# Optimization experiments

Measured on AMD Instinct MI355X. Metric: run time of the kernel, lower is better.

Reference implementation:

```python
import jax, jax.numpy as jnp
import numpy as np

K = 20  # top-K neighbors per stock
SLOPE = 0.2  # LeakyReLU negative slope


def _gru_layer(x, Wih, Whh, bih, bhh):
    # x: [N, T, D]; PyTorch GRU gate order: r, z, n
    H = Whh.shape[1]
    def step(h, xt):
        gi = xt @ Wih.T + bih            # [N, 3H]
        gh = h @ Whh.T + bhh             # [N, 3H]
        ir, iz, inn = jnp.split(gi, 3, axis=1)
        hr, hz, hn = jnp.split(gh, 3, axis=1)
        r = jax.nn.sigmoid(ir + hr)
        z = jax.nn.sigmoid(iz + hz)
        n = jnp.tanh(inn + r * hn)
        h_new = (1.0 - z) * n + z * h
        return h_new, h_new
    h0 = jnp.zeros((x.shape[0], H), x.dtype)
    _, ys = jax.lax.scan(step, h0, jnp.swapaxes(x, 0, 1))
    return jnp.swapaxes(ys, 0, 1)        # [N, T, H]


def _cos_sim(x, y):
    # torch: xy / (||x|| ||y||^T), NaN (0/0) replaced by 0
    xy = x @ y.T
    xn = jnp.sqrt(jnp.sum(x * x, axis=1, keepdims=True))
    yn = jnp.sqrt(jnp.sum(y * y, axis=1, keepdims=True))
    denom = xn @ yn.T
    safe = jnp.where(denom == 0.0, 1.0, denom)
    return jnp.where(denom == 0.0, 0.0, xy / safe)


def setup_inputs() -> dict:
    key = jax.random.key(0)
    ks = jax.random.split(key, 20)
    N, T, F, H = 4096, 64, 32, 128
    def rn(k, shape, scale=0.1):
        return jax.random.normal(k, shape, dtype=jnp.float32) * scale
    b01 = lambda n: jnp.full((n,), 0.1, jnp.float32)
    return {
        'x': jax.random.normal(ks[0], (N, T, F), dtype=jnp.float32),
        'Wih0': rn(ks[1], (3 * H, F)), 'Whh0': rn(ks[2], (3 * H, H)),
        'bih0': rn(ks[3], (3 * H,)), 'bhh0': rn(ks[4], (3 * H,)),
        'Wih1': rn(ks[5], (3 * H, H)), 'Whh1': rn(ks[6], (3 * H, H)),
        'bih1': rn(ks[7], (3 * H,)), 'bhh1': rn(ks[8], (3 * H,)),
        'W_hc': rn(ks[9], (H, H)), 'b_hc': b01(H),
        'W_hs': rn(ks[10], (H, H)), 'b_hs': b01(H),
        'W_fore': rn(ks[11], (H, H)), 'b_fore': b01(H),
        'W_back': rn(ks[12], (H, H)), 'b_back': b01(H),
        'W_indi': rn(ks[13], (H, H)), 'b_indi': b01(H),
        'W_out': rn(ks[14], (1, H)), 'b_out': b01(1),
    }


def reference(x, Wih0, Whh0, bih0, bhh0, Wih1, Whh1, bih1, bhh1,
              W_hc, b_hc, W_hs, b_hs, W_fore, b_fore, W_back, b_back,
              W_indi, b_indi, W_out, b_out):
    lrelu = lambda v: jax.nn.leaky_relu(v, SLOPE)
    h = _gru_layer(x, Wih0, Whh0, bih0, bhh0)
    h = _gru_layer(h, Wih1, Whh1, bih1, bhh1)
    g = h[:, -1, :]                                   # [N, H] last-step GRU output
    N = g.shape[0]

    sim = _cos_sim(g, g)                              # [N, N]
    diag = jnp.diagonal(sim)
    sim_off = sim * (1.0 - jnp.eye(N, dtype=sim.dtype))

    # top-K (by |sim|) neighbor mask via scatter
    cols = jax.lax.top_k(jnp.abs(sim_off), K)[1]      # [N, K]
    rows = jnp.repeat(jnp.arange(N), K)
    mask = jnp.zeros((N, N), sim.dtype).at[rows, cols.reshape(-1)].set(1.0)

    tks = sim_off * mask
    col_nz = (jnp.sum(tks, axis=0) != 0).astype(sim.dtype)
    tks = tks + jnp.diag(col_nz * diag)

    # concept features; zero rows (empty concepts) are masked instead of filtered
    concept_raw = tks.T @ g                           # [N, H]
    valid = (jnp.sum(concept_raw, axis=1) != 0).astype(g.dtype)
    cf = lrelu(concept_raw @ W_hc.T + b_hc) * valid[:, None]

    attn = jax.nn.softmax(_cos_sim(g, cf), axis=0)    # softmax over stocks per concept
    hs = lrelu((attn @ cf) @ W_hs.T + b_hs)
    back = lrelu(hs @ W_back.T + b_back)
    fore = lrelu(hs @ W_fore.T + b_fore)
    indi = lrelu((g - back) @ W_indi.T + b_indi)
    pred = (fore + indi) @ W_out.T + b_out            # [N, 1]
    return pred.squeeze(-1)
```

## Files before the change

### kernel.cpp

```cpp
#include <hip/hip_runtime.h>
#include <hip/hip_bf16.h>


typedef float f32x4 __attribute__((ext_vector_type(4)));
typedef short s16x8 __attribute__((ext_vector_type(8)));
typedef unsigned short u16;
typedef unsigned long long u64;

#define DEVFN static __device__ __forceinline__

DEVFN u16 f2bf(float f) {
  union { float f; unsigned u; } v; v.f = f;
  return (u16)((v.u + 0x7FFFu + ((v.u >> 16) & 1u)) >> 16);
}

DEVFN unsigned f2bf_pk(float lo, float hi) {
  union { __hip_bfloat162 h; unsigned u; } p;
  p.h = __float22bfloat162_rn(make_float2(lo, hi));
  return p.u;
}

DEVFN f32x4 mfma16(s16x8 a, s16x8 b, f32x4 c) {
  return __builtin_amdgcn_mfma_f32_16x16x32_bf16(a, b, c, 0, 0, 0);
}

DEVFN float sigmf(float x) { return __builtin_amdgcn_rcpf(1.f + __expf(-x)); }
DEVFN float tanhf_fast(float x) {
  float e = __expf(2.f * x);
  return 1.f - 2.f * __builtin_amdgcn_rcpf(e + 1.f);
}
DEVFN float lrelu(float v) { return v > 0.f ? v : 0.2f * v; }

__global__ void cvt_all(const float* __restrict__ w0, const float* __restrict__ w1,
                        const float* __restrict__ w2, const float* __restrict__ w3,
                        const float* __restrict__ w4, const float* __restrict__ w5,
                        const float* __restrict__ w6, const float* __restrict__ w7,
                        u16* __restrict__ dst, int* __restrict__ zbuf) {
  int i = blockIdx.x * 256 + threadIdx.x;
  if (i >= 225280) return;
  if (i < 12288) zbuf[i] = 0;
  float v;
  if      (i < 12288)  v = w0[i];
  else if (i < 61440)  v = w1[i - 12288];
  else if (i < 110592) v = w2[i - 61440];
  else if (i < 159744) v = w3[i - 110592];
  else if (i < 176128) v = w4[i - 159744];
  else if (i < 192512) v = w5[i - 176128];
  else if (i < 208896) v = w6[i - 192512];
  else                 v = w7[i - 208896];
  dst[i] = f2bf(v);
}

__launch_bounds__(512, 1)
__global__ void gru_fused(const float* __restrict__ x,
                          const u16* __restrict__ Wih0, const u16* __restrict__ Whh0,
                          const float* __restrict__ bih0, const float* __restrict__ bhh0,
                          const u16* __restrict__ Wih1, const u16* __restrict__ Whh1,
                          const float* __restrict__ bih1, const float* __restrict__ bhh1,
                          float* __restrict__ g_out, u16* __restrict__ gbf,
                          float* __restrict__ rn)
{
  const int tid  = threadIdx.x;
  const int w    = tid >> 6;
  const int l    = tid & 63;
  const int quad = l >> 4;
  const int l16  = l & 15;
  const int r0   = blockIdx.x * 16;
  const int c    = w * 16 + l16;

  __shared__ u16 sh_x[64][16 * 40];
  __shared__ u16 sh_h0[2][16 * 136];
  __shared__ u16 sh_h1[2][16 * 136];
  __shared__ float red16[16][8];

  s16x8 B0ih[3];
  s16x8 B0hh[3][4];
  s16x8 B1ih[3][4];
  s16x8 B1hh[3][4];
  float brz0[2], bin0, bhn0, brz1[2], bin1, bhn1;
  {
    int j0g = c, j1g = 128 + c, j2g = 256 + c;
    brz0[0] = bih0[j0g] + bhh0[j0g];  brz0[1] = bih0[j1g] + bhh0[j1g];
    bin0 = bih0[j2g];  bhn0 = bhh0[j2g];
    brz1[0] = bih1[j0g] + bhh1[j0g];  brz1[1] = bih1[j1g] + bhh1[j1g];
    bin1 = bih1[j2g];  bhn1 = bhh1[j2g];
  }
#pragma unroll
  for (int g = 0; g < 3; ++g) {
    int j = g * 128 + c;
    B0ih[g] = *(const s16x8*)(Wih0 + j * 32 + quad * 8);
#pragma unroll
    for (int kk = 0; kk < 4; ++kk) {
      B0hh[g][kk] = *(const s16x8*)(Whh0 + j * 128 + kk * 32 + quad * 8);
      B1ih[g][kk] = *(const s16x8*)(Wih1 + j * 128 + kk * 32 + quad * 8);
      B1hh[g][kk] = *(const s16x8*)(Whh1 + j * 128 + kk * 32 + quad * 8);
    }
  }
  float h0reg[4] = {0.f, 0.f, 0.f, 0.f};
  float h1reg[4] = {0.f, 0.f, 0.f, 0.f};
  for (int idx = tid; idx < 16 * 136; idx += 512) sh_h1[0][idx] = 0;

  for (int q = tid; q < 8192; q += 512) {
    int r  = q >> 9;
    int t  = (q >> 3) & 63;
    int c4 = (q & 7) * 4;
    float4 v = *(const float4*)(x + (size_t)(r0 + r) * 2048 + t * 32 + c4);
    unsigned p0 = f2bf_pk(v.x, v.y);
    unsigned p1 = f2bf_pk(v.z, v.w);
    *(uint2*)(&sh_x[t][r * 40 + c4]) = make_uint2(p0, p1);
  }
  __syncthreads();

  const f32x4 zz4 = {0.f, 0.f, 0.f, 0.f};
  {
    s16x8 ax = *(const s16x8*)(sh_x[0] + l16 * 40 + quad * 8);
    f32x4 ai[3];
#pragma unroll
    for (int g = 0; g < 3; ++g) ai[g] = mfma16(ax, B0ih[g], zz4);
#pragma unroll
    for (int i = 0; i < 4; i += 2) {
      float hn[2];
#pragma unroll
      for (int q = 0; q < 2; ++q) {
        int ii = i + q;
        float rr = sigmf(ai[0][ii] + brz0[0]);
        float zg = sigmf(ai[1][ii] + brz0[1]);
        float nn = tanhf_fast(ai[2][ii] + bin0 + rr * bhn0);
        hn[q] = nn - zg * nn;
        h0reg[ii] = hn[q];
      }
      unsigned pk = f2bf_pk(hn[0], hn[1]);
      int m = quad * 4 + i;
      sh_h0[0][m * 136 + c]       = (u16)pk;
      sh_h0[0][(m + 1) * 136 + c] = (u16)(pk >> 16);
    }
  }

#define GRU_STEP(T, CUR, NXT)                                                     \
  {                                                                               \
    __syncthreads();                                                              \
    s16x8 ah0[4], ah1[4];                                                         \
    _Pragma("unroll")                                                             \
    for (int kk = 0; kk < 4; ++kk) {                                              \
      ah0[kk] = *(const s16x8*)(sh_h0[CUR] + l16 * 136 + kk * 32 + quad * 8);     \
      ah1[kk] = *(const s16x8*)(sh_h1[CUR] + l16 * 136 + kk * 32 + quad * 8);     \
    }                                                                             \
    s16x8 ax = *(const s16x8*)(sh_x[(T) + 1] + l16 * 40 + quad * 8);              \
    f32x4 r1a, z1a, ni1, nh1, r0a, z0a, ni0, nh0;                                 \
    r1a = mfma16(ah0[0], B1ih[0][0], zz4);                                        \
    z1a = mfma16(ah0[0], B1ih[1][0], zz4);                                        \
    ni1 = mfma16(ah0[0], B1ih[2][0], zz4);                                        \
    nh1 = mfma16(ah1[0], B1hh[2][0], zz4);                                        \
    r0a = mfma16(ax, B0ih[0], zz4);                                               \
    z0a = mfma16(ax, B0ih[1], zz4);                                               \
    ni0 = mfma16(ax, B0ih[2], zz4);                                               \
    nh0 = mfma16(ah0[0], B0hh[2][0], zz4);                                        \
    _Pragma("unroll")                                                             \
    for (int kk = 1; kk < 4; ++kk) {                                              \
      r1a = mfma16(ah0[kk], B1ih[0][kk], r1a);                                    \
      z1a = mfma16(ah0[kk], B1ih[1][kk], z1a);                                    \
      ni1 = mfma16(ah0[kk], B1ih[2][kk], ni1);                                    \
      nh1 = mfma16(ah1[kk], B1hh[2][kk], nh1);                                    \
      nh0 = mfma16(ah0[kk], B0hh[2][kk], nh0);                                    \
    }                                                                             \
    _Pragma("unroll")                                                             \
    for (int kk = 0; kk < 4; ++kk) {                                              \
      r1a = mfma16(ah1[kk], B1hh[0][kk], r1a);                                    \
      z1a = mfma16(ah1[kk], B1hh[1][kk], z1a);                                    \
      r0a = mfma16(ah0[kk], B0hh[0][kk], r0a);                                    \
      z0a = mfma16(ah0[kk], B0hh[1][kk], z0a);                                    \
    }                                                                             \
    _Pragma("unroll")                                                             \
    for (int i = 0; i < 4; i += 2) {                                              \
      float hn[2];                                                                \
      _Pragma("unroll")                                                           \
      for (int q = 0; q < 2; ++q) {                                               \
        int ii = i + q;                                                           \
        float rr = sigmf(r1a[ii] + brz1[0]);                                      \
        float zg = sigmf(z1a[ii] + brz1[1]);                                      \
        float nn = tanhf_fast(ni1[ii] + bin1 + rr * (nh1[ii] + bhn1));            \
        hn[q] = nn + zg * (h1reg[ii] - nn);                                       \
        h1reg[ii] = hn[q];                                                        \
      }                                                                           \
      unsigned pk = f2bf_pk(hn[0], hn[1]);                                        \
      int m = quad * 4 + i;                                                       \
      sh_h1[NXT][m * 136 + c]       = (u16)pk;                                    \
      sh_h1[NXT][(m + 1) * 136 + c] = (u16)(pk >> 16);                            \
    }                                                                             \
    _Pragma("unroll")                                                             \
    for (int i = 0; i < 4; i += 2) {                                              \
      float hn[2];                                                                \
      _Pragma("unroll")                                                           \
      for (int q = 0; q < 2; ++q) {                                               \
        int ii = i + q;                                                           \
        float rr = sigmf(r0a[ii] + brz0[0]);                                      \
        float zg = sigmf(z0a[ii] + brz0[1]);                                      \
        float nn = tanhf_fast(ni0[ii] + bin0 + rr * (nh0[ii] + bhn0));            \
        hn[q] = nn + zg * (h0reg[ii] - nn);                                       \
        h0reg[ii] = hn[q];                                                        \
      }                                                                           \
      unsigned pk = f2bf_pk(hn[0], hn[1]);                                        \
      int m = quad * 4 + i;                                                       \
      sh_h0[NXT][m * 136 + c]       = (u16)pk;                                    \
      sh_h0[NXT][(m + 1) * 136 + c] = (u16)(pk >> 16);                            \
    }                                                                             \
  }

  for (int t2 = 0; t2 < 31; ++t2) {
    int t = t2 * 2;
    GRU_STEP(t, 0, 1);
    GRU_STEP(t + 1, 1, 0);
  }
  GRU_STEP(62, 0, 1);
#undef GRU_STEP

  __syncthreads();
  {
    s16x8 ah0[4], ah1[4];
#pragma unroll
    for (int kk = 0; kk < 4; ++kk) {
      ah0[kk] = *(const s16x8*)(sh_h0[1] + l16 * 136 + kk * 32 + quad * 8);
      ah1[kk] = *(const s16x8*)(sh_h1[1] + l16 * 136 + kk * 32 + quad * 8);
    }
    f32x4 r1a, z1a, ni1, nh1;
    r1a = mfma16(ah0[0], B1ih[0][0], zz4);
    z1a = mfma16(ah0[0], B1ih[1][0], zz4);
    ni1 = mfma16(ah0[0], B1ih[2][0], zz4);
    nh1 = mfma16(ah1[0], B1hh[2][0], zz4);
#pragma unroll
    for (int kk = 1; kk < 4; ++kk) {
      r1a = mfma16(ah0[kk], B1ih[0][kk], r1a);
      z1a = mfma16(ah0[kk], B1ih[1][kk], z1a);
      ni1 = mfma16(ah0[kk], B1ih[2][kk], ni1);
      nh1 = mfma16(ah1[kk], B1hh[2][kk], nh1);
    }
#pragma unroll
    for (int kk = 0; kk < 4; ++kk) {
      r1a = mfma16(ah1[kk], B1hh[0][kk], r1a);
      z1a = mfma16(ah1[kk], B1hh[1][kk], z1a);
    }
    float hv[4];
#pragma unroll
    for (int i = 0; i < 4; ++i) {
      int m = quad * 4 + i;
      float rr = sigmf(r1a[i] + brz1[0]);
      float zg = sigmf(z1a[i] + brz1[1]);
      float nn = tanhf_fast(ni1[i] + bin1 + rr * (nh1[i] + bhn1));
      float hnew = nn + zg * (h1reg[i] - nn);
      hv[i] = hnew;
      g_out[(size_t)(r0 + m) * 128 + c] = hnew;
      gbf[(size_t)(r0 + m) * 128 + c]   = f2bf(hnew);
    }
#pragma unroll
    for (int i = 0; i < 4; ++i) {
      float s = hv[i] * hv[i];
      s += __shfl_xor(s, 1);
      s += __shfl_xor(s, 2);
      s += __shfl_xor(s, 4);
      s += __shfl_xor(s, 8);
      if (l16 == 0) red16[quad * 4 + i][w] = s;
    }
  }
  __syncthreads();
  if (tid < 16) {
    float s = 0.f;
#pragma unroll
    for (int k = 0; k < 8; ++k) s += red16[tid][k];
    rn[r0 + tid] = (s == 0.f) ? 0.f : rsqrtf(s);
  }
}

template<int MODE>
__launch_bounds__(256, 1)
__global__ void cos_gemm(const u16* __restrict__ A, const u16* __restrict__ B,
                         const float* __restrict__ rnA, const float* __restrict__ rnB,
                         float* __restrict__ C, u16* __restrict__ E,
                         float* __restrict__ colsum)
{
  __shared__ u16 shA[128 * 136];
  __shared__ u16 shB[128 * 136];
  const int tid = threadIdx.x;
  const int l = tid & 63, wv = tid >> 6;
  const int quad = l >> 4, l16 = l & 15;
  const int i0 = blockIdx.y * 128, j0 = blockIdx.x * 128;
  {
    int r = tid >> 1, half = tid & 1;
    const int4* sa = (const int4*)(A + (size_t)(i0 + r) * 128 + half * 64);
    int4* da = (int4*)(shA + r * 136 + half * 64);
    const int4* sb = (const int4*)(B + (size_t)(j0 + r) * 128 + half * 64);
    int4* db = (int4*)(shB + r * 136 + half * 64);
#pragma unroll
    for (int q = 0; q < 8; ++q) { da[q] = sa[q]; db[q] = sb[q]; }
  }
  __syncthreads();
  const int wm = wv >> 1, wn = wv & 1;
  f32x4 acc[4][4];
  const f32x4 zz4 = {0.f, 0.f, 0.f, 0.f};
#pragma unroll
  for (int a = 0; a < 4; ++a)
#pragma unroll
    for (int b = 0; b < 4; ++b) acc[a][b] = zz4;
#pragma unroll
  for (int kk = 0; kk < 4; ++kk) {
    s16x8 af[4], bfr[4];
#pragma unroll
    for (int mt = 0; mt < 4; ++mt)
      af[mt] = *(const s16x8*)(shA + (wm * 64 + mt * 16 + l16) * 136 + kk * 32 + quad * 8);
#pragma unroll
    for (int nt = 0; nt < 4; ++nt)
      bfr[nt] = *(const s16x8*)(shB + (wn * 64 + nt * 16 + l16) * 136 + kk * 32 + quad * 8);
#pragma unroll
    for (int mt = 0; mt < 4; ++mt)
#pragma unroll
      for (int nt = 0; nt < 4; ++nt) acc[mt][nt] = mfma16(af[mt], bfr[nt], acc[mt][nt]);
  }
  float ra[4][4];
#pragma unroll
  for (int mt = 0; mt < 4; ++mt)
#pragma unroll
    for (int i = 0; i < 4; ++i) ra[mt][i] = rnA[i0 + wm * 64 + mt * 16 + quad * 4 + i];
#pragma unroll
  for (int nt = 0; nt < 4; ++nt) {
    int col = j0 + wn * 64 + nt * 16 + l16;
    float rb = rnB[col];
    float psum = 0.f;
#pragma unroll
    for (int mt = 0; mt < 4; ++mt)
#pragma unroll
      for (int i = 0; i < 4; ++i) {
        int row = i0 + wm * 64 + mt * 16 + quad * 4 + i;
        float v = acc[mt][nt][i] * ra[mt][i] * rb;
        if constexpr (MODE == 0) {
          C[(size_t)row * 4096 + col] = v;
        } else {
          float e = __expf(v);
          E[(size_t)row * 4096 + col] = f2bf(e);
          psum += e;
        }
      }
    if constexpr (MODE == 1) {
      psum += __shfl_xor(psum, 16);
      psum += __shfl_xor(psum, 32);
      if (quad == 0) atomicAdd(colsum + col, psum);
    }
  }
}

__launch_bounds__(256, 1)
__global__ void topk_select(const float* __restrict__ sim,
                            int* __restrict__ gselj, float* __restrict__ gselv,
                            int* __restrict__ cnt, int* __restrict__ touched)
{
  __shared__ unsigned hist[2048];
  __shared__ u64 cand[3072];
  __shared__ int selj[20];
  __shared__ unsigned ws4[4];
  __shared__ int shb, shcnt;
  const int tid = threadIdx.x;
  const int row = blockIdx.x;
  const int l = tid & 63, wv = tid >> 6;

  for (int i = tid; i < 2048; i += 256) hist[i] = 0;
  if (tid == 0) shcnt = 0;
  __syncthreads();

  unsigned key[4][4];
#pragma unroll
  for (int q = 0; q < 4; ++q) {
    int e0 = (q * 256 + tid) * 4;
    float4 v = *(const float4*)(sim + (size_t)row * 4096 + e0);
    key[q][0] = (e0 + 0 == row) ? 0u : (__float_as_uint(v.x) & 0x7FFFFFFFu);
    key[q][1] = (e0 + 1 == row) ? 0u : (__float_as_uint(v.y) & 0x7FFFFFFFu);
    key[q][2] = (e0 + 2 == row) ? 0u : (__float_as_uint(v.z) & 0x7FFFFFFFu);
    key[q][3] = (e0 + 3 == row) ? 0u : (__float_as_uint(v.w) & 0x7FFFFFFFu);
#pragma unroll
    for (int c = 0; c < 4; ++c) {
      unsigned bin = key[q][c] >> 19; if (bin > 2047u) bin = 2047u;
      atomicAdd(&hist[bin], 1u);
    }
  }
  __syncthreads();

  unsigned s = 0;
#pragma unroll
  for (int j = 0; j < 8; ++j) s += hist[tid * 8 + j];
  unsigned r = s;
#pragma unroll
  for (int off = 1; off < 64; off <<= 1) {
    unsigned o = __shfl_down(r, off);
    if (l + off < 64) r += o;
  }
  if (l == 0) ws4[wv] = r;
  __syncthreads();
  unsigned upper = 0;
  for (int q = wv + 1; q < 4; ++q) upper += ws4[q];
  unsigned excl = upper + (r - s);
  if (excl < 20u && excl + s >= 20u) {
    unsigned cum = excl;
    for (int j = 7; j >= 0; --j) {
      cum += hist[tid * 8 + j];
      if (cum >= 20u) { shb = tid * 8 + j; break; }
    }
  }
  __syncthreads();
  const unsigned b = (unsigned)shb;

#pragma unroll
  for (int q = 0; q < 4; ++q) {
    int e0 = (q * 256 + tid) * 4;
#pragma unroll
    for (int c = 0; c < 4; ++c) {
      unsigned bin = key[q][c] >> 19; if (bin > 2047u) bin = 2047u;
      if (bin >= b) {
        int p = atomicAdd(&shcnt, 1);
        if (p < 3072) cand[p] = ((u64)key[q][c] << 32) | (u64)(4095 - (e0 + c));
      }
    }
  }
  __syncthreads();
  const int C = (shcnt < 3072) ? shcnt : 3072;

  if (wv == 0) {
    for (int it = 0; it < 20; ++it) {
      u64 best = 0ull; int bpos = -1;
      for (int p = l; p < C; p += 64) {
        u64 cv = cand[p];
        if (cv > best) { best = cv; bpos = p; }
      }
      u64 mine = best;
#pragma unroll
      for (int off = 1; off < 64; off <<= 1) {
        u64 o = __shfl_xor(best, off);
        if (o > best) best = o;
      }
      if (mine == best && bpos >= 0 && best != 0ull) cand[bpos] = 0ull;
      if (l == 0) selj[it] = 4095 - (int)(best & 0xFFFull);
    }
  }
  __syncthreads();
  if (tid < 20) {
    int idx = selj[tid];
    float sv = (idx == row) ? 0.f : sim[(size_t)row * 4096 + idx];
    gselj[row * 20 + tid] = idx;
    gselv[row * 20 + tid] = sv;
    atomicAdd(&cnt[idx], 1);
    if (sv != 0.f) atomicOr(touched + idx, 1);
  }
}

__launch_bounds__(1024, 1)
__global__ void scan4096(const int* __restrict__ cnt, int* __restrict__ offs,
                         int* __restrict__ cur)
{
  __shared__ int wsum[16];
  const int t = threadIdx.x, l = t & 63, wv = t >> 6;
  int4 c = ((const int4*)cnt)[t];
  int s = c.x + c.y + c.z + c.w;
  int ps = s;
#pragma unroll
  for (int off = 1; off < 64; off <<= 1) {
    int o = __shfl_up(ps, off);
    if (l >= off) ps += o;
  }
  if (l == 63) wsum[wv] = ps;
  __syncthreads();
  if (t == 0) {
    int a = 0;
#pragma unroll
    for (int q = 0; q < 16; ++q) { int x = wsum[q]; wsum[q] = a; a += x; }
  }
  __syncthreads();
  int base = wsum[wv] + (ps - s);
  int4 o4;
  o4.x = base; o4.y = o4.x + c.x; o4.z = o4.y + c.y; o4.w = o4.z + c.z;
  ((int4*)offs)[t] = o4;
  ((int4*)cur)[t] = o4;
}

__global__ void scatter_entries(const int* __restrict__ gselj, const float* __restrict__ gselv,
                                int* __restrict__ cur, int* __restrict__ eid,
                                float* __restrict__ ev)
{
  unsigned idx = blockIdx.x * 256 + threadIdx.x;
  unsigned row = idx / 20u;
  int j = gselj[idx]; float v = gselv[idx];
  int pos = atomicAdd(&cur[j], 1);
  eid[pos] = (int)row; ev[pos] = v;
}

__launch_bounds__(128, 1)
__global__ void concept_cf(const int* __restrict__ offs, const int* __restrict__ cnt,
                           const int* __restrict__ eid, const float* __restrict__ ev,
                           const float* __restrict__ g, const float* __restrict__ rng,
                           const int* __restrict__ touched,
                           const float* __restrict__ Whc, const float* __restrict__ bhc,
                           float* __restrict__ cf, u16* __restrict__ cfbf,
                           float* __restrict__ rncf)
{
  __shared__ float shc[128];
  __shared__ float red2[2];
  const int j = blockIdx.x, d = threadIdx.x;
  const int l = d & 63, wv = d >> 6;
  const int off = offs[j], n = cnt[j];
  float acc = 0.f;
  for (int p = 0; p < n; ++p) {
    int i = eid[off + p]; float v = ev[off + p];
    acc += v * g[(size_t)i * 128 + d];
  }
  if (touched[j] && rng[j] != 0.f) acc += g[(size_t)j * 128 + d];
  float s = acc;
#pragma unroll
  for (int o = 32; o >= 1; o >>= 1) s += __shfl_xor(s, o);
  if (l == 0) red2[wv] = s;
  shc[d] = acc;
  __syncthreads();
  float valid = ((red2[0] + red2[1]) != 0.f) ? 1.f : 0.f;
  float o = bhc[d];
  const float4* wr = (const float4*)(Whc + (size_t)d * 128);
#pragma unroll 8
  for (int q = 0; q < 32; ++q) {
    float4 w4 = wr[q];
    float4 c4 = *((const float4*)shc + q);
    o += c4.x * w4.x + c4.y * w4.y + c4.z * w4.z + c4.w * w4.w;
  }
  float cfv = lrelu(o) * valid;
  cf[(size_t)j * 128 + d] = cfv;
  cfbf[(size_t)j * 128 + d] = f2bf(cfv);
  __syncthreads();
  float nn = cfv * cfv;
#pragma unroll
  for (int of = 32; of >= 1; of >>= 1) nn += __shfl_xor(nn, of);
  if (l == 0) red2[wv] = nn;
  __syncthreads();
  if (d == 0) {
    float q2 = red2[0] + red2[1];
    rncf[j] = (q2 == 0.f) ? 0.f : rsqrtf(q2);
  }
}

__global__ void scale_cfT(const float* __restrict__ cf, const float* __restrict__ colsum,
                          u16* __restrict__ cfTs)
{
  int idx = blockIdx.x * 256 + threadIdx.x;
  int n = idx >> 12, c = idx & 4095;
  float rz = __builtin_amdgcn_rcpf(colsum[c]);
  cfTs[idx] = f2bf(cf[(size_t)c * 128 + n] * rz);
}

__launch_bounds__(256, 1)
__global__ void attn_cf(const u16* __restrict__ attn, const u16* __restrict__ cfT,
                        float* __restrict__ hs_pre)
{
  __shared__ u16 shw[16 * 136];
  const int tid = threadIdx.x;
  const int l = tid & 63, wv = tid >> 6;
  const int quad = l >> 4, l16 = l & 15;
  const int r0 = blockIdx.x * 16;
  f32x4 acc[2];
  const f32x4 zz4 = {0.f, 0.f, 0.f, 0.f};
  acc[0] = zz4; acc[1] = zz4;
  for (int kc = 0; kc < 32; ++kc) {
    if (kc) __syncthreads();
    {
      int r = tid >> 4, seg = tid & 15;
      *(int4*)(shw + r * 136 + seg * 8) =
        *(const int4*)(attn + (size_t)(r0 + r) * 4096 + kc * 128 + seg * 8);
    }
    __syncthreads();
#pragma unroll
    for (int kk = 0; kk < 4; ++kk) {
      s16x8 a = *(const s16x8*)(shw + l16 * 136 + kk * 32 + quad * 8);
#pragma unroll
      for (int nt = 0; nt < 2; ++nt) {
        int n = wv * 32 + nt * 16 + l16;
        s16x8 b = *(const s16x8*)(cfT + (size_t)n * 4096 + kc * 128 + kk * 32 + quad * 8);
        acc[nt] = mfma16(a, b, acc[nt]);
      }
    }
  }
#pragma unroll
  for (int nt = 0; nt < 2; ++nt)
#pragma unroll
    for (int i = 0; i < 4; ++i) {
      int row = r0 + quad * 4 + i;
      int col = wv * 32 + nt * 16 + l16;
      hs_pre[(size_t)row * 128 + col] = acc[nt][i];
    }
}

__launch_bounds__(256, 1)
__global__ void head_kernel(const float* __restrict__ hs_pre, const float* __restrict__ g,
                            const u16* __restrict__ whs, const u16* __restrict__ wfore,
                            const u16* __restrict__ wback, const u16* __restrict__ windi,
                            const float* __restrict__ b_hs, const float* __restrict__ b_fore,
                            const float* __restrict__ b_back, const float* __restrict__ b_indi,
                            const float* __restrict__ W_out, const float* __restrict__ b_out,
                            float* __restrict__ outp)
{
  __shared__ u16 bufin[16 * 136];
  __shared__ u16 bufB[16 * 136];
  __shared__ float bufF[16 * 132];
  __shared__ float shWout[128];
  const int tid = threadIdx.x;
  const int l = tid & 63, wv = tid >> 6;
  const int quad = l >> 4, l16 = l & 15;
  const int r0 = blockIdx.x * 16;
  const f32x4 zz4 = {0.f, 0.f, 0.f, 0.f};

  if (tid < 128) shWout[tid] = W_out[tid];
  for (int idx = tid; idx < 2048; idx += 256) {
    int j = idx >> 7, n = idx & 127;
    bufin[j * 136 + n] = f2bf(hs_pre[(size_t)(r0 + j) * 128 + n]);
  }
  __syncthreads();
  {
    s16x8 a[4];
#pragma unroll
    for (int kk = 0; kk < 4; ++kk)
      a[kk] = *(const s16x8*)(bufin + l16 * 136 + kk * 32 + quad * 8);
    f32x4 acc[2]; acc[0] = zz4; acc[1] = zz4;
#pragma unroll
    for (int nt = 0; nt < 2; ++nt) {
      int n = wv * 32 + nt * 16 + l16;
#pragma unroll
      for (int kk = 0; kk < 4; ++kk)
        acc[nt] = mfma16(a[kk], *(const s16x8*)(whs + n * 128 + kk * 32 + quad * 8), acc[nt]);
    }
#pragma unroll
    for (int nt = 0; nt < 2; ++nt) {
      int n = wv * 32 + nt * 16 + l16;
      float bb = b_hs[n];
#pragma unroll
      for (int i = 0; i < 4; ++i)
        bufB[(quad * 4 + i) * 136 + n] = f2bf(lrelu(acc[nt][i] + bb));
    }
  }
  __syncthreads();
  {
    s16x8 a[4];
#pragma unroll
    for (int kk = 0; kk < 4; ++kk)
      a[kk] = *(const s16x8*)(bufB + l16 * 136 + kk * 32 + quad * 8);
    f32x4 aF[2], aB[2]; aF[0] = zz4; aF[1] = zz4; aB[0] = zz4; aB[1] = zz4;
#pragma unroll
    for (int nt = 0; nt < 2; ++nt) {
      int n = wv * 32 + nt * 16 + l16;
#pragma unroll
      for (int kk = 0; kk < 4; ++kk) {
        aF[nt] = mfma16(a[kk], *(const s16x8*)(wfore + n * 128 + kk * 32 + quad * 8), aF[nt]);
        aB[nt] = mfma16(a[kk], *(const s16x8*)(wback + n * 128 + kk * 32 + quad * 8), aB[nt]);
      }
    }
#pragma unroll
    for (int nt = 0; nt < 2; ++nt) {
      int n = wv * 32 + nt * 16 + l16;
      float bf_ = b_fore[n], bb_ = b_back[n];
#pragma unroll
      for (int i = 0; i < 4; ++i) {
        int m = quad * 4 + i;
        bufF[m * 132 + n] = lrelu(aF[nt][i] + bf_);
        float back = lrelu(aB[nt][i] + bb_);
        float gv = g[(size_t)(r0 + m) * 128 + n];
        bufin[m * 136 + n] = f2bf(gv - back);
      }
    }
  }
  __syncthreads();
  {
    s16x8 a[4];
#pragma unroll
    for (int kk = 0; kk < 4; ++kk)
      a[kk] = *(const s16x8*)(bufin + l16 * 136 + kk * 32 + quad * 8);
    f32x4 acc[2]; acc[0] = zz4; acc[1] = zz4;
#pragma unroll
    for (int nt = 0; nt < 2; ++nt) {
      int n = wv * 32 + nt * 16 + l16;
#pragma unroll
      for (int kk = 0; kk < 4; ++kk)
        acc[nt] = mfma16(a[kk], *(const s16x8*)(windi + n * 128 + kk * 32 + quad * 8), acc[nt]);
    }
#pragma unroll
    for (int nt = 0; nt < 2; ++nt) {
      int n = wv * 32 + nt * 16 + l16;
      float bi_ = b_indi[n];
#pragma unroll
      for (int i = 0; i < 4; ++i)
        bufF[(quad * 4 + i) * 132 + n] += lrelu(acc[nt][i] + bi_);
    }
  }
  __syncthreads();
  if (tid < 16) {
    float s = b_out[0];
    const float* fr = bufF + tid * 132;
    for (int n = 0; n < 128; ++n) s += fr[n] * shWout[n];
    outp[r0 + tid] = s;
  }
}

static const size_t OFF_A       = 0;
static const size_t OFF_ATTN    = 67108864;
static const size_t OFF_G       = 100663296;
static const size_t OFF_GBF     = 102760448;
static const size_t OFF_RNG     = 103809024;
static const size_t OFF_SELJ    = 103825408;
static const size_t OFF_SELV    = 104153088;
static const size_t OFF_EID     = 104480768;
static const size_t OFF_EV      = 104808448;
static const size_t OFF_CNT     = 105136128;
static const size_t OFF_TOUCH   = 105152512;
static const size_t OFF_COLSUM  = 105168896;
static const size_t OFF_OFFS    = 105185280;
static const size_t OFF_CUR     = 105201664;
static const size_t OFF_CF      = 105218048;
static const size_t OFF_CFBF    = 107315200;
static const size_t OFF_CFTS    = 108363776;
static const size_t OFF_RNCF    = 109412352;
static const size_t OFF_HSPRE   = 109428736;
static const size_t OFF_WB      = 111525888;

extern "C" void kernel_launch(void* const* d_in, const int* in_sizes, int n_in,
                              void* d_out, int out_size, void* d_ws, size_t ws_size,
                              hipStream_t stream)
{
  (void)in_sizes; (void)n_in; (void)out_size; (void)ws_size;
  const float* x      = (const float*)d_in[0];
  const float* Wih0   = (const float*)d_in[1];
  const float* Whh0   = (const float*)d_in[2];
  const float* bih0   = (const float*)d_in[3];
  const float* bhh0   = (const float*)d_in[4];
  const float* Wih1   = (const float*)d_in[5];
  const float* Whh1   = (const float*)d_in[6];
  const float* bih1   = (const float*)d_in[7];
  const float* bhh1   = (const float*)d_in[8];
  const float* W_hc   = (const float*)d_in[9];
  const float* b_hc   = (const float*)d_in[10];
  const float* W_hs   = (const float*)d_in[11];
  const float* b_hs   = (const float*)d_in[12];
  const float* W_fore = (const float*)d_in[13];
  const float* b_fore = (const float*)d_in[14];
  const float* W_back = (const float*)d_in[15];
  const float* b_back = (const float*)d_in[16];
  const float* W_indi = (const float*)d_in[17];
  const float* b_indi = (const float*)d_in[18];
  const float* W_out  = (const float*)d_in[19];
  const float* b_out  = (const float*)d_in[20];

  char* ws = (char*)d_ws;
  float* simbuf  = (float*)(ws + OFF_A);
  u16*   attnb   = (u16*)(ws + OFF_ATTN);
  float* gbuf    = (float*)(ws + OFF_G);
  u16*   gbf     = (u16*)(ws + OFF_GBF);
  float* rng     = (float*)(ws + OFF_RNG);
  int*   gselj   = (int*)(ws + OFF_SELJ);
  float* gselv   = (float*)(ws + OFF_SELV);
  int*   eid     = (int*)(ws + OFF_EID);
  float* ev      = (float*)(ws + OFF_EV);
  int*   cntb    = (int*)(ws + OFF_CNT);
  int*   touched = (int*)(ws + OFF_TOUCH);
  float* colsum  = (float*)(ws + OFF_COLSUM);
  int*   offsb   = (int*)(ws + OFF_OFFS);
  int*   curb    = (int*)(ws + OFF_CUR);
  float* cf      = (float*)(ws + OFF_CF);
  u16*   cfbf    = (u16*)(ws + OFF_CFBF);
  u16*   cfTs    = (u16*)(ws + OFF_CFTS);
  float* rncf    = (float*)(ws + OFF_RNCF);
  float* hs_pre  = (float*)(ws + OFF_HSPRE);
  u16*   wsB     = (u16*)(ws + OFF_WB);
  u16 *wih0b = wsB, *whh0b = wsB + 12288, *wih1b = wsB + 61440, *whh1b = wsB + 110592;
  u16 *whsb = wsB + 159744, *wforeb = wsB + 176128, *wbackb = wsB + 192512, *windib = wsB + 208896;

  cvt_all<<<880, 256, 0, stream>>>(Wih0, Whh0, Wih1, Whh1, W_hs, W_fore, W_back, W_indi,
                                   wsB, cntb);

  gru_fused<<<256, 512, 0, stream>>>(x, wih0b, whh0b, bih0, bhh0,
                                     wih1b, whh1b, bih1, bhh1, gbuf, gbf, rng);

  cos_gemm<0><<<dim3(32, 32), 256, 0, stream>>>(gbf, gbf, rng, rng, simbuf,
                                                (u16*)nullptr, (float*)nullptr);

  topk_select<<<4096, 256, 0, stream>>>(simbuf, gselj, gselv, cntb, touched);
  scan4096<<<1, 1024, 0, stream>>>(cntb, offsb, curb);
  scatter_entries<<<320, 256, 0, stream>>>(gselj, gselv, curb, eid, ev);
  concept_cf<<<4096, 128, 0, stream>>>(offsb, cntb, eid, ev, gbuf, rng, touched,
                                       W_hc, b_hc, cf, cfbf, rncf);

  cos_gemm<1><<<dim3(32, 32), 256, 0, stream>>>(gbf, cfbf, rng, rncf, (float*)nullptr,
                                                attnb, colsum);
  scale_cfT<<<2048, 256, 0, stream>>>(cf, colsum, cfTs);
  attn_cf<<<256, 256, 0, stream>>>(attnb, cfTs, hs_pre);

  head_kernel<<<256, 256, 0, stream>>>(hs_pre, gbuf, whsb, wforeb, wbackb, windib,
                                       b_hs, b_fore, b_back, b_indi, W_out, b_out,
                                       (float*)d_out);
}
```

Measured before the change: 429.6 us.

## Use adaptive min/max histogram bins in top-k and tile the cf transpose

The top-k selection now computes each row's min and max key and spreads the 2048 histogram bins over that range, instead of using fixed exponent-based bins. This is meant to shrink the candidate set, and a single-register warp path handles the case of 64 or fewer candidates. The scale_cfT transpose now goes through a shared-memory tile so both global reads and writes are coalesced, with fewer blocks. The new binning adds a block-wide reduction and float binning, which could cause ties or precision problems at bin edges.

```diff
diff --git a/kernel.cpp b/kernel.cpp
--- a/kernel.cpp
+++ b/kernel.cpp
@@ -355,6 +355,7 @@
   __shared__ u64 cand[3072];
   __shared__ int selj[20];
   __shared__ unsigned ws4[4];
+  __shared__ unsigned wmin4[4], wmax4[4];
   __shared__ int shb, shcnt;
   const int tid = threadIdx.x;
   const int row = blockIdx.x;
@@ -362,9 +363,9 @@
 
   for (int i = tid; i < 2048; i += 256) hist[i] = 0;
   if (tid == 0) shcnt = 0;
-  __syncthreads();
 
   unsigned key[4][4];
+  unsigned lmin = 0xFFFFFFFFu, lmax = 0u;
 #pragma unroll
   for (int q = 0; q < 4; ++q) {
     int e0 = (q * 256 + tid) * 4;
@@ -375,10 +376,31 @@
     key[q][3] = (e0 + 3 == row) ? 0u : (__float_as_uint(v.w) & 0x7FFFFFFFu);
 #pragma unroll
     for (int c = 0; c < 4; ++c) {
-      unsigned bin = key[q][c] >> 19; if (bin > 2047u) bin = 2047u;
+      unsigned k = key[q][c];
+      lmin = k < lmin ? k : lmin;
+      lmax = k > lmax ? k : lmax;
+    }
+  }
+#pragma unroll
+  for (int off = 1; off < 64; off <<= 1) {
+    unsigned om = __shfl_xor(lmin, off); lmin = om < lmin ? om : lmin;
+    unsigned ox = __shfl_xor(lmax, off); lmax = ox > lmax ? ox : lmax;
+  }
+  if (l == 0) { wmin4[wv] = lmin; wmax4[wv] = lmax; }
+  __syncthreads();
+  const unsigned kmin = min(min(wmin4[0], wmin4[1]), min(wmin4[2], wmin4[3]));
+  const unsigned kmax = max(max(wmax4[0], wmax4[1]), max(wmax4[2], wmax4[3]));
+  const float binscale = (kmax > kmin) ? (2047.0f / (float)(kmax - kmin)) : 0.0f;
+
+#define BIN_OF(k) ((int)((float)((k) - kmin) * binscale))
+
+#pragma unroll
+  for (int q = 0; q < 4; ++q)
+#pragma unroll
+    for (int c = 0; c < 4; ++c) {
+      int bin = BIN_OF(key[q][c]); if (bin > 2047) bin = 2047;
       atomicAdd(&hist[bin], 1u);
     }
-  }
   __syncthreads();
 
   unsigned s = 0;
@@ -403,38 +425,53 @@
     }
   }
   __syncthreads();
-  const unsigned b = (unsigned)shb;
+  const int b = shb;
 
 #pragma unroll
   for (int q = 0; q < 4; ++q) {
     int e0 = (q * 256 + tid) * 4;
 #pragma unroll
     for (int c = 0; c < 4; ++c) {
-      unsigned bin = key[q][c] >> 19; if (bin > 2047u) bin = 2047u;
+      int bin = BIN_OF(key[q][c]); if (bin > 2047) bin = 2047;
       if (bin >= b) {
         int p = atomicAdd(&shcnt, 1);
         if (p < 3072) cand[p] = ((u64)key[q][c] << 32) | (u64)(4095 - (e0 + c));
       }
     }
   }
+#undef BIN_OF
   __syncthreads();
   const int C = (shcnt < 3072) ? shcnt : 3072;
 
   if (wv == 0) {
-    for (int it = 0; it < 20; ++it) {
-      u64 best = 0ull; int bpos = -1;
-      for (int p = l; p < C; p += 64) {
-        u64 cv = cand[p];
-        if (cv > best) { best = cv; bpos = p; }
+    if (C <= 64) {
+      u64 mykey = (l < C) ? cand[l] : 0ull;
+      for (int it = 0; it < 20; ++it) {
+        u64 m = mykey;
+#pragma unroll
+        for (int off = 1; off < 64; off <<= 1) {
+          u64 o = __shfl_xor(m, off);
+          if (o > m) m = o;
+        }
+        if (mykey == m) mykey = 0ull;
+        if (l == 0) selj[it] = 4095 - (int)(m & 0xFFFull);
       }
-      u64 mine = best;
-#pragma unroll
-      for (int off = 1; off < 64; off <<= 1) {
-        u64 o = __shfl_xor(best, off);
-        if (o > best) best = o;
+    } else {
+      for (int it = 0; it < 20; ++it) {
+        u64 best = 0ull; int bpos = -1;
+        for (int p = l; p < C; p += 64) {
+          u64 cv = cand[p];
+          if (cv > best) { best = cv; bpos = p; }
+        }
+        u64 mine = best;
+#pragma unroll
+        for (int off = 1; off < 64; off <<= 1) {
+          u64 o = __shfl_xor(best, off);
+          if (o > best) best = o;
+        }
+        if (mine == best && bpos >= 0 && best != 0ull) cand[bpos] = 0ull;
+        if (l == 0) selj[it] = 4095 - (int)(best & 0xFFFull);
       }
-      if (mine == best && bpos >= 0 && best != 0ull) cand[bpos] = 0ull;
-      if (l == 0) selj[it] = 4095 - (int)(best & 0xFFFull);
     }
   }
   __syncthreads();
@@ -538,13 +575,37 @@
   }
 }
 
+__launch_bounds__(256, 1)
 __global__ void scale_cfT(const float* __restrict__ cf, const float* __restrict__ colsum,
                           u16* __restrict__ cfTs)
 {
-  int idx = blockIdx.x * 256 + threadIdx.x;
-  int n = idx >> 12, c = idx & 4095;
-  float rz = __builtin_amdgcn_rcpf(colsum[c]);
-  cfTs[idx] = f2bf(cf[(size_t)c * 128 + n] * rz);
+  __shared__ float tile[32][132];
+  __shared__ float rz[32];
+  const int t = threadIdx.x;
+  const int c0 = blockIdx.x * 32;
+  if (t < 32) rz[t] = __builtin_amdgcn_rcpf(colsum[c0 + t]);
+#pragma unroll
+  for (int k = 0; k < 4; ++k) {
+    int lin = k * 256 + t;
+    int r = lin >> 5;
+    int q = lin & 31;
+    float4 v = *(const float4*)(cf + (size_t)(c0 + r) * 128 + q * 4);
+    tile[r][q * 4 + 0] = v.x; tile[r][q * 4 + 1] = v.y;
+    tile[r][q * 4 + 2] = v.z; tile[r][q * 4 + 3] = v.w;
+  }
+  __syncthreads();
+#pragma unroll
+  for (int k = 0; k < 4; ++k) {
+    int lin = k * 256 + t;
+    int n  = lin >> 3;
+    int c4 = (lin & 7) * 4;
+    ushort4 o;
+    o.x = f2bf(tile[c4 + 0][n] * rz[c4 + 0]);
+    o.y = f2bf(tile[c4 + 1][n] * rz[c4 + 1]);
+    o.z = f2bf(tile[c4 + 2][n] * rz[c4 + 2]);
+    o.w = f2bf(tile[c4 + 3][n] * rz[c4 + 3]);
+    *(ushort4*)(cfTs + (size_t)n * 4096 + c0 + c4) = o;
+  }
 }
 
 __launch_bounds__(256, 1)
@@ -786,7 +847,7 @@
 
   cos_gemm<1><<<dim3(32, 32), 256, 0, stream>>>(gbf, cfbf, rng, rncf, (float*)nullptr,
                                                 attnb, colsum);
-  scale_cfT<<<2048, 256, 0, stream>>>(cf, colsum, cfTs);
+  scale_cfT<<<128, 256, 0, stream>>>(cf, colsum, cfTs);
   attn_cf<<<256, 256, 0, stream>>>(attnb, cfTs, hs_pre);
 
   head_kernel<<<256, 256, 0, stream>>>(hs_pre, gbuf, whsb, wforeb, wbackb, windib,
```

Measured after the change: 429.3 us. About the same (-0.1%).
